# Performance work log

Hardware: AMD Instinct MI355X
Metric: run time of the kernel (lower is better)

Reference implementation:

```python
import jax, jax.numpy as jnp
import numpy as np

TIMESCALE = 10.0   # NeuralODE init kwarg
N_MAX = 48         # static upper bound on number of constant-size Dopri5 steps
B, D, H = 8192, 128, 128


def _mlp(y, W1, b1, W2, b2):
    # autonomous dynamics f(x): tanh MLP, applied along last dim
    return jnp.tanh(y @ W1 + b1) @ W2 + b2


def _dopri5_step(y, dt, f):
    # classic Dormand-Prince 5(4) tableau; autonomous f, so c_i unused
    k1 = f(y)
    k2 = f(y + dt * (1.0 / 5.0 * k1))
    k3 = f(y + dt * (3.0 / 40.0 * k1 + 9.0 / 40.0 * k2))
    k4 = f(y + dt * (44.0 / 45.0 * k1 - 56.0 / 15.0 * k2 + 32.0 / 9.0 * k3))
    k5 = f(y + dt * (19372.0 / 6561.0 * k1 - 25360.0 / 2187.0 * k2
                     + 64448.0 / 6561.0 * k3 - 212.0 / 729.0 * k4))
    k6 = f(y + dt * (9017.0 / 3168.0 * k1 - 355.0 / 33.0 * k2
                     + 46732.0 / 5247.0 * k3 + 49.0 / 176.0 * k4
                     - 5103.0 / 18656.0 * k5))
    return y + dt * (35.0 / 384.0 * k1 + 500.0 / 1113.0 * k3
                     + 125.0 / 192.0 * k4 - 2187.0 / 6784.0 * k5
                     + 11.0 / 84.0 * k6)


def _initial_step_size(y0, f0, f, order=4, rtol=1.4e-8, atol=1.4e-8):
    # faithful port of NeuralODE.initial_step_size (Hairer heuristic)
    scale = atol + jnp.abs(y0) * rtol
    d0 = jnp.linalg.norm(y0 / scale)
    d1 = jnp.linalg.norm(f0 / scale)
    h0 = jnp.where((d0 < 1e-5) | (d1 < 1e-5), 1e-6, 0.01 * d0 / d1)
    y1 = y0 + h0 * f0
    f1 = f(y1)
    d2 = jnp.linalg.norm((f1 - f0) / scale) / h0
    h1 = jnp.where((d1 <= 1e-15) & (d2 <= 1e-15),
                   jnp.maximum(1e-6, h0 * 1e-3),
                   (0.01 / (d1 + d2)) ** (1.0 / (order + 1.0)))
    return jnp.minimum(100.0 * h0, h1)


def setup_inputs() -> dict:
    key = jax.random.key(0)
    k0, k1, k2 = jax.random.split(key, 3)
    x = jax.random.normal(k0, (B, D), jnp.float32)
    W1 = jax.random.normal(k1, (D, H), jnp.float32) * (1.0 / D ** 0.5)
    b1 = jnp.zeros((H,), jnp.float32)
    W2 = jax.random.normal(k2, (H, D), jnp.float32) * (1.0 / H ** 0.5)
    b2 = jnp.zeros((D,), jnp.float32)
    t = jnp.ones((1,), jnp.float32)
    return {"t": t, "x": x, "W1": W1, "b1": b1, "W2": W2, "b2": b2}


def reference(t, x, W1, b1, W2, b2):
    f = lambda y: _mlp(y, W1, b1, W2, b2)
    # dt0 from the first state row, exactly as the original (x[0, :])
    dt0 = _initial_step_size(x[0], f(x[0]), f)
    T = t[0] / TIMESCALE  # linspace(0, t/timescale, 2) -> ts = [0, T]

    # diffrax default ConstantStepSize: fixed-dt Dopri5 until t reaches T.
    # Static-length scan with dt clamped to the remaining interval; once
    # t == T, dt == 0 and the step is skipped via lax.cond.
    step = jax.checkpoint(
        lambda y, dt: jax.lax.cond(dt > 0.0,
                                   lambda a: _dopri5_step(a, dt, f),
                                   lambda a: a, y))

    def body(carry, _):
        tt, y = carry
        dt = jnp.clip(T - tt, 0.0, dt0)
        return (tt + dt, step(y, dt)), None

    (_, yT), _ = jax.lax.scan(body, (jnp.zeros((), jnp.float32), x), None,
                              length=N_MAX)
    # SaveAt(ts=[0, T]) -> ys has leading axis n_samples=2
    return jnp.stack([x, yT])
```

## Files before the change

kernel.cpp:

```cpp
#include <hip/hip_runtime.h>


typedef __attribute__((ext_vector_type(8))) short short8;
typedef __attribute__((ext_vector_type(4))) float f32x4;

#define SL 136

__device__ __forceinline__ short f2bf(float f) {
  union { float f; unsigned u; } v; v.f = f;
  return (short)((v.u + 0x8000u) >> 16);
}

__device__ __forceinline__ float fast_tanh(float x) {
  float e = __expf(2.0f * x);
  return 1.0f - __fdividef(2.0f, e + 1.0f);
}

__global__ __launch_bounds__(256, 2)
void node_kernel(const float* __restrict__ tptr, const float* __restrict__ x,
                 const float* __restrict__ W1, const float* __restrict__ b1,
                 const float* __restrict__ W2, const float* __restrict__ b2,
                 float* __restrict__ out) {
  const int tid  = threadIdx.x;
  const int wv   = tid >> 6;
  const int lane = tid & 63;
  const int q    = lane >> 4;
  const int colL = lane & 15;
  const int blockRow = blockIdx.x * 16;

  __shared__ short A1[16][SL];
  __shared__ short A2[16][SL];
  __shared__ float sred[256];
  __shared__ float spart[2][128];
  __shared__ float srowY[128], srowH[128], srowF[128], srowY2[128], srowF2[128], sscale[128];

  short8 w1f[2][4], w2f[2][4];
  float b1v[2], b2v[2];
  int ncol[2];
#pragma unroll
  for (int j = 0; j < 2; ++j) {
    const int n = (2 * wv + j) * 16 + colL;
    ncol[j] = n;
    b1v[j] = b1[n]; b2v[j] = b2[n];
#pragma unroll
    for (int kt = 0; kt < 4; ++kt) {
      short8 v1, v2;
#pragma unroll
      for (int i = 0; i < 8; ++i) {
        const int k = kt * 32 + q * 8 + i;
        v1[i] = f2bf(W1[k * 128 + n]);
        v2[i] = f2bf(W2[k * 128 + n]);
      }
      w1f[j][kt] = v1; w2f[j][kt] = v2;
    }
  }

  auto block_sum = [&](float v) -> float {
    sred[tid] = v;
    __syncthreads();
    if (tid < 64) {
      float s = sred[tid] + sred[tid + 64] + sred[tid + 128] + sred[tid + 192];
#pragma unroll
      for (int o = 32; o > 0; o >>= 1) s += __shfl_down(s, o, 64);
      if (tid == 0) sred[0] = s;
    }
    __syncthreads();
    float r = sred[0];
    __syncthreads();
    return r;
  };

  auto mlp_layer = [&](const float* vin, const float* Wg, const float* bg,
                       float* vout, bool dotanh) {
    const int col = tid & 127, part = tid >> 7;
    float s = 0.f;
    const float* wp = Wg + (part * 64) * 128 + col;
#pragma unroll 8
    for (int j = 0; j < 64; ++j) s += vin[part * 64 + j] * wp[j * 128];
    spart[part][col] = s;
    __syncthreads();
    if (tid < 128) {
      float a = bg[tid] + spart[0][tid] + spart[1][tid];
      vout[tid] = dotanh ? fast_tanh(a) : a;
    }
    __syncthreads();
  };

  if (tid < 128) srowY[tid] = x[tid];
  __syncthreads();
  mlp_layer(srowY, W1, b1, srowH, true);
  mlp_layer(srowH, W2, b2, srowF, false);
  float t0 = 0.f, t1 = 0.f;
  if (tid < 128) {
    float sc = 1.4e-8f + fabsf(srowY[tid]) * 1.4e-8f;
    sscale[tid] = sc;
    float a = srowY[tid] / sc; t0 = a * a;
    float bq = srowF[tid] / sc; t1 = bq * bq;
  }
  float d0 = sqrtf(block_sum(t0));
  float d1 = sqrtf(block_sum(t1));
  float h0 = (d0 < 1e-5f || d1 < 1e-5f) ? 1e-6f : 0.01f * d0 / d1;
  if (tid < 128) srowY2[tid] = srowY[tid] + h0 * srowF[tid];
  __syncthreads();
  mlp_layer(srowY2, W1, b1, srowH, true);
  mlp_layer(srowH, W2, b2, srowF2, false);
  float t2 = 0.f;
  if (tid < 128) { float a = (srowF2[tid] - srowF[tid]) / sscale[tid]; t2 = a * a; }
  float d2 = sqrtf(block_sum(t2)) / h0;
  float h1 = (d1 <= 1e-15f && d2 <= 1e-15f) ? fmaxf(1e-6f, h0 * 1e-3f)
                                            : powf(0.01f / (d1 + d2), 0.2f);
  const float dt0v = fminf(100.f * h0, h1);

  f32x4 yr[2];
#pragma unroll
  for (int j = 0; j < 2; ++j)
#pragma unroll
    for (int r = 0; r < 4; ++r)
      yr[j][r] = x[(blockRow + q * 4 + r) * 128 + ncol[j]];

  short* const wr1 = &A1[q * 4][0];
  short* const wr2 = &A2[q * 4][0];
  const short* const rd1 = &A1[colL][q * 8];
  const short* const rd2 = &A2[colL][q * 8];

  auto evalF = [&](auto&& gen, f32x4 (&fout)[2]) {
#pragma unroll
    for (int j = 0; j < 2; ++j) {
      f32x4 v = gen(j);
#pragma unroll
      for (int r = 0; r < 4; ++r) wr1[r * SL + ncol[j]] = f2bf(v[r]);
    }
    __syncthreads();
    short8 af[4];
#pragma unroll
    for (int kt = 0; kt < 4; ++kt) af[kt] = *(const short8*)(rd1 + kt * 32);
    f32x4 acc0 = {b1v[0], b1v[0], b1v[0], b1v[0]};
    f32x4 acc1 = {b1v[1], b1v[1], b1v[1], b1v[1]};
    __builtin_amdgcn_s_setprio(1);
#pragma unroll
    for (int kt = 0; kt < 4; ++kt) {
      acc0 = __builtin_amdgcn_mfma_f32_16x16x32_bf16(af[kt], w1f[0][kt], acc0, 0, 0, 0);
      acc1 = __builtin_amdgcn_mfma_f32_16x16x32_bf16(af[kt], w1f[1][kt], acc1, 0, 0, 0);
    }
    __builtin_amdgcn_s_setprio(0);
#pragma unroll
    for (int r = 0; r < 4; ++r) wr2[r * SL + ncol[0]] = f2bf(fast_tanh(acc0[r]));
#pragma unroll
    for (int r = 0; r < 4; ++r) wr2[r * SL + ncol[1]] = f2bf(fast_tanh(acc1[r]));
    __syncthreads();
#pragma unroll
    for (int kt = 0; kt < 4; ++kt) af[kt] = *(const short8*)(rd2 + kt * 32);
    f32x4 f0 = {b2v[0], b2v[0], b2v[0], b2v[0]};
    f32x4 f1 = {b2v[1], b2v[1], b2v[1], b2v[1]};
    __builtin_amdgcn_s_setprio(1);
#pragma unroll
    for (int kt = 0; kt < 4; ++kt) {
      f0 = __builtin_amdgcn_mfma_f32_16x16x32_bf16(af[kt], w2f[0][kt], f0, 0, 0, 0);
      f1 = __builtin_amdgcn_mfma_f32_16x16x32_bf16(af[kt], w2f[1][kt], f1, 0, 0, 0);
    }
    __builtin_amdgcn_s_setprio(0);
    fout[0] = f0; fout[1] = f1;
  };

  const float T = tptr[0] / 10.0f;
  float tt = 0.f;
  f32x4 k1[2], k2[2], k3[2], k4[2], k5[2], k6[2];

#pragma unroll 1
  for (int it = 0; it < 48; ++it) {
    float dt = fminf(fmaxf(T - tt, 0.f), dt0v);
    if (dt <= 0.f) break;
    evalF([&](int j) { return yr[j]; }, k1);
    {
      const float c1 = dt * 0.2f;
      evalF([&](int j) { return yr[j] + c1 * k1[j]; }, k2);
    }
    {
      const float c1 = dt * 0.075f, c2 = dt * 0.225f;
      evalF([&](int j) { return yr[j] + c1 * k1[j] + c2 * k2[j]; }, k3);
    }
    {
      const float c1 = dt * 0.9777777777777777f, c2 = dt * -3.7333333333333334f,
                  c3 = dt * 3.5555555555555554f;
      evalF([&](int j) { return yr[j] + c1 * k1[j] + c2 * k2[j] + c3 * k3[j]; }, k4);
    }
    {
      const float c1 = dt * 2.9525986892242035f, c2 = dt * -11.595793324188385f,
                  c3 = dt * 9.822892851699436f, c4 = dt * -0.2908093278463649f;
      evalF([&](int j) {
        return yr[j] + c1 * k1[j] + c2 * k2[j] + c3 * k3[j] + c4 * k4[j];
      }, k5);
    }
    {
      const float c1 = dt * 2.8462752525252526f, c2 = dt * -10.757575757575758f,
                  c3 = dt * 8.906422717743473f, c4 = dt * 0.2784090909090909f,
                  c5 = dt * -0.27351165254237287f;
      evalF([&](int j) {
        return yr[j] + c1 * k1[j] + c2 * k2[j] + c3 * k3[j] + c4 * k4[j]
                     + c5 * k5[j];
      }, k6);
    }
    {
      const float c1 = dt * 0.0911458333333333f, c3 = dt * 0.449236298292902f,
                  c4 = dt * 0.6510416666666666f, c5 = dt * -0.32237617924528303f,
                  c6 = dt * 0.13095238095238096f;
#pragma unroll
      for (int j = 0; j < 2; ++j)
        yr[j] = yr[j] + c1 * k1[j] + c3 * k3[j] + c4 * k4[j] + c5 * k5[j]
                      + c6 * k6[j];
    }
    tt += dt;
  }

  {
    const float4* x4 = (const float4*)(x + blockRow * 128);
    float4* o4 = (float4*)(out + blockRow * 128);
    o4[tid] = x4[tid];
    o4[tid + 256] = x4[tid + 256];
    float* oy = out + 8192 * 128;
#pragma unroll
    for (int j = 0; j < 2; ++j)
#pragma unroll
      for (int r = 0; r < 4; ++r)
        oy[(blockRow + q * 4 + r) * 128 + ncol[j]] = yr[j][r];
  }
}

extern "C" void kernel_launch(void* const* d_in, const int* in_sizes, int n_in,
                              void* d_out, int out_size, void* d_ws, size_t ws_size,
                              hipStream_t stream) {
  const float* t  = (const float*)d_in[0];
  const float* x  = (const float*)d_in[1];
  const float* W1 = (const float*)d_in[2];
  const float* b1 = (const float*)d_in[3];
  const float* W2 = (const float*)d_in[4];
  const float* b2 = (const float*)d_in[5];
  float* out = (float*)d_out;
  node_kernel<<<dim3(512), dim3(256), 0, stream>>>(t, x, W1, b1, W2, b2, out);
}
```

Measured before the change: 164.0 us.

## Compute dt0 with MFMA evalF, use hardware exp2/rcp tanh and packed bf16 conversion

The scalar fp32 GEMV used for the initial step-size heuristic is replaced by the same bf16 MFMA evalF path, with the single row x[0] broadcast across the tile. This removes global weight reads and extra barriers from the prologue. fast_tanh now uses the native exp2 and rcp instructions, and bf16 conversion uses v_cvt_pk_bf16_f32 to pack two values at once. The trade-off is that dt0 is now computed from bf16-rounded matmuls, which may shift the step size slightly away from the fp32 reference.

Measured after the change: 138.7 us (median of 2 runs). 1.18x faster.

```diff
diff --git a/kernel.cpp b/kernel.cpp
--- a/kernel.cpp
+++ b/kernel.cpp
@@ -12,8 +12,17 @@
 }
 
 __device__ __forceinline__ float fast_tanh(float x) {
-  float e = __expf(2.0f * x);
-  return 1.0f - __fdividef(2.0f, e + 1.0f);
+  float e = __builtin_amdgcn_exp2f(x * 2.88539008177793f);
+  float r = __builtin_amdgcn_rcpf(e + 1.0f);
+  return __builtin_fmaf(-2.0f, r, 1.0f);
+}
+
+__device__ __forceinline__ void store_bf16_pair(short* p0, short* p1,
+                                                float a, float b) {
+  unsigned u;
+  asm("v_cvt_pk_bf16_f32 %0, %1, %2" : "=v"(u) : "v"(a), "v"(b));
+  *p0 = (short)(u & 0xffffu);
+  *p1 = (short)(u >> 16);
 }
 
 __global__ __launch_bounds__(256, 2)
@@ -31,8 +40,6 @@
   __shared__ short A1[16][SL];
   __shared__ short A2[16][SL];
   __shared__ float sred[256];
-  __shared__ float spart[2][128];
-  __shared__ float srowY[128], srowH[128], srowF[128], srowY2[128], srowF2[128], sscale[128];
 
   short8 w1f[2][4], w2f[2][4];
   float b1v[2], b2v[2];
@@ -70,42 +77,84 @@
     return r;
   };
 
-  auto mlp_layer = [&](const float* vin, const float* Wg, const float* bg,
-                       float* vout, bool dotanh) {
-    const int col = tid & 127, part = tid >> 7;
-    float s = 0.f;
-    const float* wp = Wg + (part * 64) * 128 + col;
-#pragma unroll 8
-    for (int j = 0; j < 64; ++j) s += vin[part * 64 + j] * wp[j * 128];
-    spart[part][col] = s;
-    __syncthreads();
-    if (tid < 128) {
-      float a = bg[tid] + spart[0][tid] + spart[1][tid];
-      vout[tid] = dotanh ? fast_tanh(a) : a;
-    }
-    __syncthreads();
+  short* const wr1 = &A1[q * 4][0];
+  short* const wr2 = &A2[q * 4][0];
+  const short* const rd1 = &A1[colL][q * 8];
+  const short* const rd2 = &A2[colL][q * 8];
+
+  auto evalF = [&](auto&& gen, f32x4 (&fout)[2]) {
+#pragma unroll
+    for (int j = 0; j < 2; ++j) {
+      f32x4 v = gen(j);
+      store_bf16_pair(&wr1[0 * SL + ncol[j]], &wr1[1 * SL + ncol[j]], v[0], v[1]);
+      store_bf16_pair(&wr1[2 * SL + ncol[j]], &wr1[3 * SL + ncol[j]], v[2], v[3]);
+    }
+    __syncthreads();
+    short8 af[4];
+#pragma unroll
+    for (int kt = 0; kt < 4; ++kt) af[kt] = *(const short8*)(rd1 + kt * 32);
+    f32x4 acc0 = {b1v[0], b1v[0], b1v[0], b1v[0]};
+    f32x4 acc1 = {b1v[1], b1v[1], b1v[1], b1v[1]};
+    __builtin_amdgcn_s_setprio(1);
+#pragma unroll
+    for (int kt = 0; kt < 4; ++kt) {
+      acc0 = __builtin_amdgcn_mfma_f32_16x16x32_bf16(af[kt], w1f[0][kt], acc0, 0, 0, 0);
+      acc1 = __builtin_amdgcn_mfma_f32_16x16x32_bf16(af[kt], w1f[1][kt], acc1, 0, 0, 0);
+    }
+    __builtin_amdgcn_s_setprio(0);
+    {
+      float h0a = fast_tanh(acc0[0]), h1a = fast_tanh(acc0[1]);
+      float h2a = fast_tanh(acc0[2]), h3a = fast_tanh(acc0[3]);
+      store_bf16_pair(&wr2[0 * SL + ncol[0]], &wr2[1 * SL + ncol[0]], h0a, h1a);
+      store_bf16_pair(&wr2[2 * SL + ncol[0]], &wr2[3 * SL + ncol[0]], h2a, h3a);
+      float h0b = fast_tanh(acc1[0]), h1b = fast_tanh(acc1[1]);
+      float h2b = fast_tanh(acc1[2]), h3b = fast_tanh(acc1[3]);
+      store_bf16_pair(&wr2[0 * SL + ncol[1]], &wr2[1 * SL + ncol[1]], h0b, h1b);
+      store_bf16_pair(&wr2[2 * SL + ncol[1]], &wr2[3 * SL + ncol[1]], h2b, h3b);
+    }
+    __syncthreads();
+#pragma unroll
+    for (int kt = 0; kt < 4; ++kt) af[kt] = *(const short8*)(rd2 + kt * 32);
+    f32x4 f0 = {b2v[0], b2v[0], b2v[0], b2v[0]};
+    f32x4 f1 = {b2v[1], b2v[1], b2v[1], b2v[1]};
+    __builtin_amdgcn_s_setprio(1);
+#pragma unroll
+    for (int kt = 0; kt < 4; ++kt) {
+      f0 = __builtin_amdgcn_mfma_f32_16x16x32_bf16(af[kt], w2f[0][kt], f0, 0, 0, 0);
+      f1 = __builtin_amdgcn_mfma_f32_16x16x32_bf16(af[kt], w2f[1][kt], f1, 0, 0, 0);
+    }
+    __builtin_amdgcn_s_setprio(0);
+    fout[0] = f0; fout[1] = f1;
   };
 
-  if (tid < 128) srowY[tid] = x[tid];
-  __syncthreads();
-  mlp_layer(srowY, W1, b1, srowH, true);
-  mlp_layer(srowH, W2, b2, srowF, false);
+  float y0j[2], scl[2];
+#pragma unroll
+  for (int j = 0; j < 2; ++j) {
+    y0j[j] = x[ncol[j]];
+    scl[j] = 1.4e-8f + fabsf(y0j[j]) * 1.4e-8f;
+  }
+  f32x4 fb[2];
+  evalF([&](int j) { float v = y0j[j]; return (f32x4){v, v, v, v}; }, fb);
+  float f0j[2] = {fb[0][0], fb[1][0]};
   float t0 = 0.f, t1 = 0.f;
-  if (tid < 128) {
-    float sc = 1.4e-8f + fabsf(srowY[tid]) * 1.4e-8f;
-    sscale[tid] = sc;
-    float a = srowY[tid] / sc; t0 = a * a;
-    float bq = srowF[tid] / sc; t1 = bq * bq;
+  if (q == 0) {
+#pragma unroll
+    for (int j = 0; j < 2; ++j) {
+      float a = y0j[j] / scl[j]; t0 += a * a;
+      float b = f0j[j] / scl[j]; t1 += b * b;
+    }
   }
   float d0 = sqrtf(block_sum(t0));
   float d1 = sqrtf(block_sum(t1));
   float h0 = (d0 < 1e-5f || d1 < 1e-5f) ? 1e-6f : 0.01f * d0 / d1;
-  if (tid < 128) srowY2[tid] = srowY[tid] + h0 * srowF[tid];
-  __syncthreads();
-  mlp_layer(srowY2, W1, b1, srowH, true);
-  mlp_layer(srowH, W2, b2, srowF2, false);
+  evalF([&](int j) { float v = y0j[j] + h0 * f0j[j]; return (f32x4){v, v, v, v}; }, fb);
   float t2 = 0.f;
-  if (tid < 128) { float a = (srowF2[tid] - srowF[tid]) / sscale[tid]; t2 = a * a; }
+  if (q == 0) {
+#pragma unroll
+    for (int j = 0; j < 2; ++j) {
+      float a = (fb[j][0] - f0j[j]) / scl[j]; t2 += a * a;
+    }
+  }
   float d2 = sqrtf(block_sum(t2)) / h0;
   float h1 = (d1 <= 1e-15f && d2 <= 1e-15f) ? fmaxf(1e-6f, h0 * 1e-3f)
                                             : powf(0.01f / (d1 + d2), 0.2f);
@@ -117,50 +166,6 @@
 #pragma unroll
     for (int r = 0; r < 4; ++r)
       yr[j][r] = x[(blockRow + q * 4 + r) * 128 + ncol[j]];
-
-  short* const wr1 = &A1[q * 4][0];
-  short* const wr2 = &A2[q * 4][0];
-  const short* const rd1 = &A1[colL][q * 8];
-  const short* const rd2 = &A2[colL][q * 8];
-
-  auto evalF = [&](auto&& gen, f32x4 (&fout)[2]) {
-#pragma unroll
-    for (int j = 0; j < 2; ++j) {
-      f32x4 v = gen(j);
-#pragma unroll
-      for (int r = 0; r < 4; ++r) wr1[r * SL + ncol[j]] = f2bf(v[r]);
-    }
-    __syncthreads();
-    short8 af[4];
-#pragma unroll
-    for (int kt = 0; kt < 4; ++kt) af[kt] = *(const short8*)(rd1 + kt * 32);
-    f32x4 acc0 = {b1v[0], b1v[0], b1v[0], b1v[0]};
-    f32x4 acc1 = {b1v[1], b1v[1], b1v[1], b1v[1]};
-    __builtin_amdgcn_s_setprio(1);
-#pragma unroll
-    for (int kt = 0; kt < 4; ++kt) {
-      acc0 = __builtin_amdgcn_mfma_f32_16x16x32_bf16(af[kt], w1f[0][kt], acc0, 0, 0, 0);
-      acc1 = __builtin_amdgcn_mfma_f32_16x16x32_bf16(af[kt], w1f[1][kt], acc1, 0, 0, 0);
-    }
-    __builtin_amdgcn_s_setprio(0);
-#pragma unroll
-    for (int r = 0; r < 4; ++r) wr2[r * SL + ncol[0]] = f2bf(fast_tanh(acc0[r]));
-#pragma unroll
-    for (int r = 0; r < 4; ++r) wr2[r * SL + ncol[1]] = f2bf(fast_tanh(acc1[r]));
-    __syncthreads();
-#pragma unroll
-    for (int kt = 0; kt < 4; ++kt) af[kt] = *(const short8*)(rd2 + kt * 32);
-    f32x4 f0 = {b2v[0], b2v[0], b2v[0], b2v[0]};
-    f32x4 f1 = {b2v[1], b2v[1], b2v[1], b2v[1]};
-    __builtin_amdgcn_s_setprio(1);
-#pragma unroll
-    for (int kt = 0; kt < 4; ++kt) {
-      f0 = __builtin_amdgcn_mfma_f32_16x16x32_bf16(af[kt], w2f[0][kt], f0, 0, 0, 0);
-      f1 = __builtin_amdgcn_mfma_f32_16x16x32_bf16(af[kt], w2f[1][kt], f1, 0, 0, 0);
-    }
-    __builtin_amdgcn_s_setprio(0);
-    fout[0] = f0; fout[1] = f1;
-  };
 
   const float T = tptr[0] / 10.0f;
   float tt = 0.f;
```
